# Kernel optimization log

Measured on AMD Instinct MI355X. Metric: run time of the kernel, lower is better.

The kernel has to match this reference:

```python
import jax, jax.numpy as jnp
import numpy as np

B = 2048      # seed nodes per batch
F1, F2 = 10, 25  # fanouts
D = 128       # combined dense feature dim
H = 256       # hidden_dim
N = 1 + F1 + F1 * F2  # 261 hop-ordered sampled nodes per seed


def setup_inputs() -> dict:
    key = jax.random.key(0)
    k1, k2, k3 = jax.random.split(key, 3)
    x = jax.random.normal(k1, (B, N, D), dtype=jnp.float32)
    W1 = jax.random.normal(k2, (2 * D, H), dtype=jnp.float32) / np.sqrt(2.0 * D)
    b1 = jnp.zeros((H,), dtype=jnp.float32)
    W2 = jax.random.normal(k3, (2 * H, H), dtype=jnp.float32) / np.sqrt(2.0 * H)
    b2 = jnp.zeros((H,), dtype=jnp.float32)
    return {"x": x, "W1": W1, "b1": b1, "W2": W2, "b2": b2}


def _sage(src, neigh_mean, W, b):
    # concat(self, mean(neighbors)) -> dense : GraphSAGE mean aggregator
    return jnp.concatenate([src, neigh_mean], axis=-1) @ W + b


def reference(x, W1, b1, W2, b2):
    # split hop-ordered flat features into bipartite blocks
    seeds = x[:, :1, :]                         # [B, 1, D]   hop0
    hop1 = x[:, 1:1 + F1, :]                    # [B, F1, D]  hop1
    hop2 = x[:, 1 + F1:, :].reshape(B, F1, F2, D)  # [B, F1, F2, D] hop2

    # SAGE layer 1 (relu): update hop0 and hop1 nodes
    h0 = jax.nn.relu(_sage(seeds, jnp.mean(hop1, axis=1, keepdims=True), W1, b1))  # [B, 1, H]
    h1 = jax.nn.relu(_sage(hop1, jnp.mean(hop2, axis=2), W1, b1))                  # [B, F1, H]

    # SAGE layer 2 (no activation): update hop0 from hop1
    out = _sage(h0, jnp.mean(h1, axis=1, keepdims=True), W2, b2)  # [B, 1, H]
    # matches tf.squeeze(src_feature [B,1,1,H], axis=2) -> [B, 1, H]
    return out
```

## Files before the change

### kernel.cpp

```cpp
#include <hip/hip_runtime.h>


#define NB 2048
#define F1 10
#define F2 25
#define DD 128
#define HH 256
#define NN 261
#define ITEMS 4
#define THREADS 256

typedef __attribute__((ext_vector_type(8))) short short8;
typedef __attribute__((ext_vector_type(4))) float f32x4;

__device__ __forceinline__ ushort f2bf(float f) {
    unsigned u = __builtin_bit_cast(unsigned, f);
    u = (u + 0x7FFFu + ((u >> 16) & 1u)) >> 16;
    return (ushort)u;
}
__device__ __forceinline__ float bf2f(ushort h) {
    unsigned u = ((unsigned)h) << 16;
    return __builtin_bit_cast(float, u);
}
__device__ __forceinline__ int swz(int uidx, int row) {
    return uidx ^ ((row & 7) << 3);
}

__global__ __launch_bounds__(256)
void prep_weights(const float* __restrict__ W1, const float* __restrict__ W2,
                  ushort* __restrict__ W1t, ushort* __restrict__ W2t)
{
    __shared__ float tile[32][65];
    const int b = blockIdx.x, t = threadIdx.x;
    const float* src; ushort* dst; int K, c0, k0;
    if (b < 32) { src = W1; dst = W1t; K = 2 * DD;
                  c0 = (b & 7) * 32; k0 = (b >> 3) * 64; }
    else { int bb = b - 32; src = W2; dst = W2t; K = 2 * HH;
           c0 = (bb & 7) * 32; k0 = (bb >> 3) * 64; }

    #pragma unroll
    for (int kr = 0; kr < 8; ++kr) {
        int kl = kr * 8 + (t >> 5);
        tile[t & 31][kl] = src[(size_t)(k0 + kl) * HH + c0 + (t & 31)];
    }
    __syncthreads();
    const int cl = t >> 3, kc = t & 7;
    short8 v;
    #pragma unroll
    for (int i = 0; i < 8; ++i) v[i] = (short)f2bf(tile[cl][kc * 8 + i]);
    *reinterpret_cast<short8*>(dst + (size_t)(c0 + cl) * K + k0 + kc * 8) = v;
}

__global__ __launch_bounds__(THREADS)
void sage_fused(const float* __restrict__ x, const ushort* __restrict__ W1t,
                const ushort* __restrict__ W2t, const float* __restrict__ b1,
                const float* __restrict__ b2, float* __restrict__ out)
{
    __shared__ ushort featL[ITEMS * 16 * 256];
    __shared__ ushort f2lds[16][520];

    const int t = threadIdx.x;
    const int item0 = blockIdx.x * ITEMS;
    const size_t base = (size_t)item0 * (NN * DD);

    {
        const int g = t >> 5, d4 = t & 31;
        #pragma unroll
        for (int p = 0; p < 5; ++p) {
            int pi = g + p * 8;
            int item = pi / 10, f = pi % 10;
            const float4* xb = reinterpret_cast<const float4*>(x + base + (size_t)item * (NN * DD));
            float4 h1 = xb[(1 + f) * 32 + d4];
            float4 s = make_float4(0.f, 0.f, 0.f, 0.f);
            const float4* h2 = xb + (1 + F1 + f * F2) * 32 + d4;
            #pragma unroll
            for (int j = 0; j < F2; ++j) {
                float4 v = h2[j * 32];
                s.x += v.x; s.y += v.y; s.z += v.z; s.w += v.w;
            }
            const float invF2 = 1.f / F2;
            int row = 1 + f;
            int ub = (item * 16 + row) * 256;
            ushort4 lo = { f2bf(h1.x), f2bf(h1.y), f2bf(h1.z), f2bf(h1.w) };
            ushort4 hi = { f2bf(s.x * invF2), f2bf(s.y * invF2),
                           f2bf(s.z * invF2), f2bf(s.w * invF2) };
            *reinterpret_cast<ushort4*>(&featL[swz(ub + d4 * 4, row)]) = lo;
            *reinterpret_cast<ushort4*>(&featL[swz(ub + DD + d4 * 4, row)]) = hi;
        }
    }
    __syncthreads();

    #pragma unroll
    for (int q = 0; q < 2; ++q) {
        int idx = t + q * 256;
        int item = idx >> 7, d = idx & 127;
        int r0 = item * 16 * 256;
        float sv = x[base + (size_t)item * (NN * DD) + d];
        featL[swz(r0 + d, 0)] = f2bf(sv);
        float m = 0.f;
        #pragma unroll
        for (int f = 1; f <= F1; ++f) m += bf2f(featL[swz(r0 + f * 256 + d, f)]);
        featL[swz(r0 + DD + d, 0)] = f2bf(m * (1.f / F1));
    }
    {
        short8 zz = { 0, 0, 0, 0, 0, 0, 0, 0 };
        for (int z = t; z < ITEMS * 5 * 32; z += THREADS) {
            int item = z / 160, rem = z % 160;
            int row = 11 + rem / 32, kc = rem % 32;
            *reinterpret_cast<short8*>(&featL[swz((item * 16 + row) * 256 + kc * 8, row)]) = zz;
        }
        for (int z = t; z < 12 * 64; z += THREADS) {
            int row = ITEMS + (z >> 6), kc = z & 63;
            *reinterpret_cast<short8*>(&f2lds[row][kc * 8]) = zz;
        }
    }
    __syncthreads();

    const int w = t >> 6, l = t & 63;
    const int lr = l & 15, lg = l >> 4;
    f32x4 acc[ITEMS][4];
    #pragma unroll
    for (int it = 0; it < ITEMS; ++it)
        #pragma unroll
        for (int i = 0; i < 4; ++i) acc[it][i] = (f32x4){0.f, 0.f, 0.f, 0.f};

    #pragma unroll 2
    for (int kt = 0; kt < 8; ++kt) {
        short8 af[ITEMS], bf[4];
        #pragma unroll
        for (int it = 0; it < ITEMS; ++it)
            af[it] = *reinterpret_cast<const short8*>(
                &featL[swz((it * 16 + lr) * 256 + kt * 32 + lg * 8, lr)]);
        #pragma unroll
        for (int i = 0; i < 4; ++i) {
            int col = (w * 4 + i) * 16 + lr;
            bf[i] = *reinterpret_cast<const short8*>(W1t + (size_t)col * 256 + kt * 32 + lg * 8);
        }
        #pragma unroll
        for (int it = 0; it < ITEMS; ++it)
            #pragma unroll
            for (int i = 0; i < 4; ++i)
                acc[it][i] = __builtin_amdgcn_mfma_f32_16x16x32_bf16(af[it], bf[i], acc[it][i], 0, 0, 0);
    }

    #pragma unroll
    for (int i = 0; i < 4; ++i) {
        const int col = (w * 4 + i) * 16 + lr;
        const float bb = b1[col];
        #pragma unroll
        for (int it = 0; it < ITEMS; ++it) {
            f32x4 a = acc[it][i];
            float r0v = fmaxf(a[0] + bb, 0.f);
            float r1v = fmaxf(a[1] + bb, 0.f);
            float r2v = fmaxf(a[2] + bb, 0.f);
            float r3v = fmaxf(a[3] + bb, 0.f);
            const int rb = lg * 4;
            float p = 0.f;
            p += (rb + 0 >= 1 && rb + 0 <= 10) ? r0v : 0.f;
            p += (rb + 1 >= 1 && rb + 1 <= 10) ? r1v : 0.f;
            p += (rb + 2 >= 1 && rb + 2 <= 10) ? r2v : 0.f;
            p += (rb + 3 >= 1 && rb + 3 <= 10) ? r3v : 0.f;
            p += __shfl_xor(p, 16, 64);
            p += __shfl_xor(p, 32, 64);
            if (lg == 0) {
                f2lds[it][col]       = f2bf(r0v);
                f2lds[it][256 + col] = f2bf(p * (1.f / F1));
            }
        }
    }
    __syncthreads();

    f32x4 acc2[4];
    #pragma unroll
    for (int i = 0; i < 4; ++i) acc2[i] = (f32x4){0.f, 0.f, 0.f, 0.f};
    #pragma unroll 2
    for (int kt = 0; kt < 16; ++kt) {
        short8 a2 = *reinterpret_cast<const short8*>(&f2lds[lr][kt * 32 + lg * 8]);
        #pragma unroll
        for (int i = 0; i < 4; ++i) {
            int col = (w * 4 + i) * 16 + lr;
            short8 bv = *reinterpret_cast<const short8*>(W2t + (size_t)col * 512 + kt * 32 + lg * 8);
            acc2[i] = __builtin_amdgcn_mfma_f32_16x16x32_bf16(a2, bv, acc2[i], 0, 0, 0);
        }
    }
    #pragma unroll
    for (int i = 0; i < 4; ++i) {
        const int col = (w * 4 + i) * 16 + lr;
        const float bb = b2[col];
        #pragma unroll
        for (int r = 0; r < 4; ++r) {
            const int row = lg * 4 + r;
            if (row < ITEMS)
                out[(size_t)(item0 + row) * HH + col] = acc2[i][r] + bb;
        }
    }
}

extern "C" void kernel_launch(void* const* d_in, const int* in_sizes, int n_in,
                              void* d_out, int out_size, void* d_ws, size_t ws_size,
                              hipStream_t stream) {
    const float* x  = (const float*)d_in[0];
    const float* W1 = (const float*)d_in[1];
    const float* b1 = (const float*)d_in[2];
    const float* W2 = (const float*)d_in[3];
    const float* b2 = (const float*)d_in[4];
    float* out = (float*)d_out;

    ushort* W1t = (ushort*)d_ws;
    ushort* W2t = W1t + 256 * 256;

    prep_weights<<<dim3(96), dim3(256), 0, stream>>>(W1, W2, W1t, W2t);
    sage_fused<<<dim3(NB / ITEMS), dim3(THREADS), 0, stream>>>(x, W1t, W2t, b1, b2, out);
}
```

Before: 71.30 us.

## Split second SAGE GEMM into separate kernel with full 16-row MFMA tiles

Unfuses the layer-2 GEMM from the feature kernel. The feature kernel now writes the bf16 layer-2 inputs (h0 and the mean of h1) to a global workspace. A new kernel then runs the 512x256 GEMM over 16 items per block, so all MFMA rows are used instead of 4 of 16. This removes the wasted MFMA work and the extra LDS and sync in the fused kernel, at the cost of another launch and a global round trip of a small intermediate.

```diff
diff --git a/kernel.cpp b/kernel.cpp
--- a/kernel.cpp
+++ b/kernel.cpp
@@ -52,12 +52,10 @@
 }
 
 __global__ __launch_bounds__(THREADS)
-void sage_fused(const float* __restrict__ x, const ushort* __restrict__ W1t,
-                const ushort* __restrict__ W2t, const float* __restrict__ b1,
-                const float* __restrict__ b2, float* __restrict__ out)
+void sage_feat(const float* __restrict__ x, const ushort* __restrict__ W1t,
+               const float* __restrict__ b1, ushort* __restrict__ f2g)
 {
     __shared__ ushort featL[ITEMS * 16 * 256];
-    __shared__ ushort f2lds[16][520];
 
     const int t = threadIdx.x;
     const int item0 = blockIdx.x * ITEMS;
@@ -109,10 +107,6 @@
             int row = 11 + rem / 32, kc = rem % 32;
             *reinterpret_cast<short8*>(&featL[swz((item * 16 + row) * 256 + kc * 8, row)]) = zz;
         }
-        for (int z = t; z < 12 * 64; z += THREADS) {
-            int row = ITEMS + (z >> 6), kc = z & 63;
-            *reinterpret_cast<short8*>(&f2lds[row][kc * 8]) = zz;
-        }
     }
     __syncthreads();
 
@@ -163,24 +157,37 @@
             p += __shfl_xor(p, 16, 64);
             p += __shfl_xor(p, 32, 64);
             if (lg == 0) {
-                f2lds[it][col]       = f2bf(r0v);
-                f2lds[it][256 + col] = f2bf(p * (1.f / F1));
+                ushort* fr = f2g + (size_t)(item0 + it) * 512;
+                fr[col]       = f2bf(r0v);
+                fr[256 + col] = f2bf(p * (1.f / F1));
             }
         }
     }
-    __syncthreads();
-
-    f32x4 acc2[4];
-    #pragma unroll
-    for (int i = 0; i < 4; ++i) acc2[i] = (f32x4){0.f, 0.f, 0.f, 0.f};
+}
+
+__global__ __launch_bounds__(256)
+void sage_gemm2(const ushort* __restrict__ f2g, const ushort* __restrict__ W2t,
+                const float* __restrict__ b2, float* __restrict__ out)
+{
+    const int t = threadIdx.x;
+    const int w = t >> 6, l = t & 63;
+    const int lr = l & 15, lg = l >> 4;
+    const int m0 = blockIdx.x * 16;
+
+    f32x4 acc[4];
+    #pragma unroll
+    for (int i = 0; i < 4; ++i) acc[i] = (f32x4){0.f, 0.f, 0.f, 0.f};
+
     #pragma unroll 2
     for (int kt = 0; kt < 16; ++kt) {
-        short8 a2 = *reinterpret_cast<const short8*>(&f2lds[lr][kt * 32 + lg * 8]);
+        short8 af = *reinterpret_cast<const short8*>(
+            f2g + (size_t)(m0 + lr) * 512 + kt * 32 + lg * 8);
         #pragma unroll
         for (int i = 0; i < 4; ++i) {
             int col = (w * 4 + i) * 16 + lr;
-            short8 bv = *reinterpret_cast<const short8*>(W2t + (size_t)col * 512 + kt * 32 + lg * 8);
-            acc2[i] = __builtin_amdgcn_mfma_f32_16x16x32_bf16(a2, bv, acc2[i], 0, 0, 0);
+            short8 bv = *reinterpret_cast<const short8*>(
+                W2t + (size_t)col * 512 + kt * 32 + lg * 8);
+            acc[i] = __builtin_amdgcn_mfma_f32_16x16x32_bf16(af, bv, acc[i], 0, 0, 0);
         }
     }
     #pragma unroll
@@ -190,8 +197,7 @@
         #pragma unroll
         for (int r = 0; r < 4; ++r) {
             const int row = lg * 4 + r;
-            if (row < ITEMS)
-                out[(size_t)(item0 + row) * HH + col] = acc2[i][r] + bb;
+            out[(size_t)(m0 + row) * HH + col] = acc[i][r] + bb;
         }
     }
 }
@@ -208,7 +214,9 @@
 
     ushort* W1t = (ushort*)d_ws;
     ushort* W2t = W1t + 256 * 256;
+    ushort* f2g = W2t + 256 * 512;
 
     prep_weights<<<dim3(96), dim3(256), 0, stream>>>(W1, W2, W1t, W2t);
-    sage_fused<<<dim3(NB / ITEMS), dim3(THREADS), 0, stream>>>(x, W1t, W2t, b1, b2, out);
-}
+    sage_feat<<<dim3(NB / ITEMS), dim3(THREADS), 0, stream>>>(x, W1t, b1, f2g);
+    sage_gemm2<<<dim3(NB / 16), dim3(256), 0, stream>>>(f2g, W2t, b2, out);
+}
```

After: 67.82 us, median of 2. -4.9%, faster.
